# Performance work log

Hardware: AMD Instinct MI355X
Metric: run time of the kernel (lower is better)

## Reference

```python
import jax, jax.numpy as jnp
import numpy as np

K = 16  # neighbors
EPS = 1e-5

def conv1x1(x, w):
    # x: (B,C,N,1), w: (O,C) -> (B,O,N,1)
    return jnp.einsum('oc,bcnw->bonw', w, x)

def batch_norm(x, gamma, beta):
    # training-mode BatchNorm2d: biased batch stats over (B,N,W)
    mean = jnp.mean(x, axis=(0, 2, 3), keepdims=True)
    var = jnp.var(x, axis=(0, 2, 3), keepdims=True)
    xn = (x - mean) * jax.lax.rsqrt(var + EPS)
    return xn * gamma[None, :, None, None] + beta[None, :, None, None]

def gelu(x):
    return jax.nn.gelu(x, approximate=False)  # torch exact GELU

def knn_idx(x, k):
    # x: (B,C,N,1) -> neighbor indices (B,N,k), no grad (detach in torch)
    feat = jnp.squeeze(x, -1).transpose(0, 2, 1)  # (B,N,C)
    sq = jnp.sum(feat * feat, axis=-1)            # (B,N)
    dist = sq[:, :, None] - 2.0 * jnp.einsum('bnc,bmc->bnm', feat, feat) + sq[:, None, :]
    _, idx = jax.lax.top_k(-dist, k)              # nearest k (B,N,k)
    return idx

def mr_conv(x, idx, w, b, gamma, beta):
    # MRConv2d: x_j = gather neighbors, aggregate max(x_j - x_i), interleave channels, 1x1 conv + BN + GELU
    B, C, N, _ = x.shape
    feat = jnp.squeeze(x, -1)  # (B,C,N)
    # x_j[b,c,n,m] = feat[b,c,idx[b,n,m]]
    x_j = jax.vmap(lambda f, i: f[:, i])(feat, idx)      # (B,C,N,k)
    agg = jnp.max(x_j - feat[:, :, :, None], axis=-1)    # (B,C,N)
    # cat([x.unsqueeze(2), x_j.unsqueeze(2)], dim=2).reshape(B, 2C, N, 1) -> interleaved channels
    h = jnp.stack([feat, agg], axis=2).reshape(B, 2 * C, N)[..., None]  # (B,2C,N,1)
    h = jnp.einsum('oc,bcnw->bonw', w, h) + b[None, :, None, None]
    return gelu(batch_norm(h, gamma, beta))

def setup_inputs() -> dict:
    key = jax.random.key(0)
    ks = jax.random.split(key, 5)
    B, C, N = 4, 192, 4096
    s = 1.0 / np.sqrt(C)
    return {
        'x': jax.random.normal(ks[0], (B, C, N, 1), jnp.float32),
        'w_fc1': jax.random.normal(ks[1], (C, C), jnp.float32) * s,
        'w_fc2': jax.random.normal(ks[2], (C, C), jnp.float32) * s,
        'w_mr': jax.random.normal(ks[3], (C, 2 * C), jnp.float32) * (1.0 / np.sqrt(2 * C)),
        'b_mr': jnp.zeros((C,), jnp.float32),
        'g0': jnp.ones((C,), jnp.float32), 'b0': jnp.zeros((C,), jnp.float32),
        'gm': jnp.ones((C,), jnp.float32), 'bm': jnp.zeros((C,), jnp.float32),
        'g1': jnp.ones((C,), jnp.float32), 'b1': jnp.zeros((C,), jnp.float32),
    }

def reference(x, w_fc1, w_fc2, w_mr, b_mr, g0, b0, gm, bm, g1, b1):
    inp = x
    h = batch_norm(conv1x1(x, w_fc1), g0, b0)
    idx = knn_idx(jax.lax.stop_gradient(h), K)
    h = mr_conv(h, idx, w_mr, b_mr, gm, bm)
    h = batch_norm(gelu(h), g1, b1)
    h = conv1x1(h, w_fc2)
    return h + inp
```

## Files before the change

### kernel.cpp

```cpp
#include <hip/hip_runtime.h>
#include <hip/hip_bf16.h>
#include <math.h>

#define BSZ 4
#define NPT 4096
#define CH  192
#define KNB 16
#define KPH 16
#define KCAND (2 * KPH)
#define NTOT ((float)(BSZ * NPT))
#define NT64 ((double)(BSZ * NPT))

typedef short short8 __attribute__((ext_vector_type(8)));
typedef float f32x4  __attribute__((ext_vector_type(4)));

__device__ __forceinline__ float gelu_exact(float x){
    return 0.5f * x * (1.0f + erff(x * 0.70710678118654752440f));
}
__device__ __forceinline__ unsigned int umin_(unsigned int a, unsigned int b){ return a < b ? a : b; }
__device__ __forceinline__ unsigned int umax_(unsigned int a, unsigned int b){ return a < b ? b : a; }
__device__ __forceinline__ unsigned int umed3_(unsigned int a, unsigned int b, unsigned int c){
    unsigned int r;
    asm("v_med3_u32 %0, %1, %2, %3" : "=v"(r) : "v"(a), "v"(b), "v"(c));
    return r;
}
__device__ __forceinline__ unsigned short bf16rnd(float v){
    unsigned int bits = __builtin_bit_cast(unsigned int, v);
    return (unsigned short)((bits + 0x7fff + ((bits >> 16) & 1)) >> 16);
}

__global__ __launch_bounds__(256) void k_fc1_f64(
    const float* __restrict__ in, const float* __restrict__ W, double* __restrict__ outd,
    double* __restrict__ s0sum, double* __restrict__ s0sq)
{
    constexpr int OT = 8, NT = 4;
    __shared__ float wtT[CH][OT];
    __shared__ double redS[4][8], redQ[4][8];
    const int tid = threadIdx.x;
    const int o0  = blockIdx.y * OT;
    const int b   = blockIdx.z;
    const int n   = blockIdx.x * (256 * NT) + tid * NT;

    for (int lin = tid; lin < CH * OT; lin += 256){
        int c = lin >> 3, o = lin & 7;
        wtT[c][o] = W[(size_t)(o0 + o) * CH + c];
    }
    __syncthreads();

    double acc[OT][NT] = {};
    const float* ip = in + (size_t)b * CH * NPT + n;
    for (int c = 0; c < CH; ++c){
        float4 x4 = *reinterpret_cast<const float4*>(ip + (size_t)c * NPT);
        double xv[NT] = {x4.x, x4.y, x4.z, x4.w};
        float4 w0 = *reinterpret_cast<const float4*>(&wtT[c][0]);
        float4 w1 = *reinterpret_cast<const float4*>(&wtT[c][4]);
        double wv[OT] = {w0.x, w0.y, w0.z, w0.w, w1.x, w1.y, w1.z, w1.w};
        #pragma unroll
        for (int oo = 0; oo < OT; ++oo)
            #pragma unroll
            for (int j = 0; j < NT; ++j)
                acc[oo][j] = fma(wv[oo], xv[j], acc[oo][j]);
    }

    double ps[OT], pq[OT];
    #pragma unroll
    for (int oo = 0; oo < OT; ++oo){
        size_t off = ((size_t)b * CH + o0 + oo) * NPT + n;
        double s = 0., q = 0.;
        #pragma unroll
        for (int j = 0; j < 4; ++j){
            double v = acc[oo][j];
            outd[off + j] = v;
            s += v; q = fma(v, v, q);
        }
        ps[oo] = s; pq[oo] = q;
    }

    #pragma unroll
    for (int oo = 0; oo < OT; ++oo){
        #pragma unroll
        for (int off = 32; off; off >>= 1){
            ps[oo] += __shfl_xor(ps[oo], off);
            pq[oo] += __shfl_xor(pq[oo], off);
        }
    }
    const int wv = tid >> 6, lane = tid & 63;
    if (lane == 0){
        #pragma unroll
        for (int oo = 0; oo < OT; ++oo){ redS[wv][oo] = ps[oo]; redQ[wv][oo] = pq[oo]; }
    }
    __syncthreads();
    if (tid < 8){
        double s = redS[0][tid] + redS[1][tid] + redS[2][tid] + redS[3][tid];
        double q = redQ[0][tid] + redQ[1][tid] + redQ[2][tid] + redQ[3][tid];
        atomicAdd(&s0sum[o0 + tid], s);
        atomicAdd(&s0sq[o0 + tid], q);
    }
}

__global__ void k_feat(
    const double* __restrict__ t1d, const float* __restrict__ g0,
    const double* __restrict__ s0sum, const double* __restrict__ s0sq,
    double* __restrict__ featT, float* __restrict__ feat32,
    unsigned short* __restrict__ featP, float* __restrict__ sqv)
{
    __shared__ double tile[32][33];
    __shared__ float sqp[32][33];
    __shared__ double scdl[CH];
    const int n0 = blockIdx.x * 32, b = blockIdx.y;
    const int tx = threadIdx.x, ty = threadIdx.y;
    const int tid = ty * 32 + tx;
    float part[4] = {0.f, 0.f, 0.f, 0.f};
    unsigned short* fpb = featP + (size_t)b * NPT * CH;

    for (int i = tid; i < CH; i += 256){
        double mean = s0sum[i] / NT64;
        double var  = s0sq[i] / NT64 - mean * mean;
        scdl[i] = (1.0 / sqrt(var + 1e-5)) * (double)g0[i];
    }
    __syncthreads();

    for (int cc = 0; cc < CH / 32; ++cc){
        const int cbase = cc * 32;
        #pragma unroll
        for (int r = 0; r < 32; r += 8){
            int c = cbase + ty + r;
            tile[ty + r][tx] = t1d[((size_t)b * CH + c) * NPT + n0 + tx] * scdl[c];
        }
        __syncthreads();
        #pragma unroll
        for (int r = 0; r < 32; r += 8){
            int n = n0 + ty + r;
            int c = cbase + tx;
            double v = tile[tx][ty + r];
            size_t o = ((size_t)b * NPT + n) * CH + c;
            featT[o] = v;
            float f = (float)v;
            feat32[o] = f;
            part[r >> 3] = fmaf(f, f, part[r >> 3]);
        }
        if (tid < 128){
            const int t_ = tid >> 6;
            const int l  = tid & 63;
            const int r_ = l & 15, g_ = l >> 4;
            const int nl = t_ * 16 + r_;
            short8 pk;
            #pragma unroll
            for (int e = 0; e < 8; ++e)
                pk[e] = (short)bf16rnd((float)tile[g_ * 8 + e][nl]);
            const int tP = blockIdx.x * 2 + t_;
            *reinterpret_cast<short8*>(fpb + (size_t)(tP * 6 + cc) * 512 + l * 8) = pk;
        }
        __syncthreads();
    }
    #pragma unroll
    for (int j = 0; j < 4; ++j) sqp[ty + 8 * j][tx] = part[j];
    __syncthreads();
    if (ty == 0){
        float s = 0.f;
        #pragma unroll 8
        for (int k = 0; k < 32; ++k) s += sqp[tx][k];
        sqv[b * NPT + n0 + tx] = s;
    }
}

__global__ __launch_bounds__(1024, 8) void k_knn_mfma(
    const unsigned short* __restrict__ featP, const float* __restrict__ sqv,
    int* __restrict__ idxh)
{
    __shared__ unsigned int mlist[16][16][17];
    const int tid  = threadIdx.x;
    const int wv   = tid >> 6;
    const int lane = tid & 63;
    const int r = lane & 15, g = lane >> 4;
    const int b    = blockIdx.y;
    const int qt   = blockIdx.x >> 1;
    const int half = blockIdx.x & 1;
    const int qs = wv >> 2, me = wv & 3;
    const int tq   = qt * 4 + qs;
    const int tm0  = half * 128 + me * 32;
    const unsigned short* fp = featP + (size_t)b * NPT * CH;

    short8 bq0, bq1, bq2, bq3, bq4, bq5;
    {
        const unsigned short* qp = fp + (size_t)tq * 3072 + lane * 8;
        bq0 = *reinterpret_cast<const short8*>(qp);
        bq1 = *reinterpret_cast<const short8*>(qp + 512);
        bq2 = *reinterpret_cast<const short8*>(qp + 1024);
        bq3 = *reinterpret_cast<const short8*>(qp + 1536);
        bq4 = *reinterpret_cast<const short8*>(qp + 2048);
        bq5 = *reinterpret_cast<const short8*>(qp + 2560);
    }

    unsigned int Q[16];
    #pragma unroll
    for (int e = 0; e < 16; ++e) Q[e] = 0xFFFFFFFFu;

    const float* sq = sqv + b * NPT;
    const unsigned short* pa = fp + (size_t)tm0 * 3072 + lane * 8;

    for (int it = 0; it < 32; ++it){
        const unsigned short* p = pa + (size_t)it * 3072;
        short8 a0 = *reinterpret_cast<const short8*>(p);
        short8 a1 = *reinterpret_cast<const short8*>(p + 512);
        short8 a2 = *reinterpret_cast<const short8*>(p + 1024);
        short8 a3 = *reinterpret_cast<const short8*>(p + 1536);
        short8 a4 = *reinterpret_cast<const short8*>(p + 2048);
        short8 a5 = *reinterpret_cast<const short8*>(p + 2560);
        const int tm = tm0 + it;
        float4 s4 = *reinterpret_cast<const float4*>(sq + tm * 16 + 4 * g);

        f32x4 acc = {0.f, 0.f, 0.f, 0.f};
        acc = __builtin_amdgcn_mfma_f32_16x16x32_bf16(a0, bq0, acc, 0, 0, 0);
        acc = __builtin_amdgcn_mfma_f32_16x16x32_bf16(a1, bq1, acc, 0, 0, 0);
        acc = __builtin_amdgcn_mfma_f32_16x16x32_bf16(a2, bq2, acc, 0, 0, 0);
        acc = __builtin_amdgcn_mfma_f32_16x16x32_bf16(a3, bq3, acc, 0, 0, 0);
        acc = __builtin_amdgcn_mfma_f32_16x16x32_bf16(a4, bq4, acc, 0, 0, 0);
        acc = __builtin_amdgcn_mfma_f32_16x16x32_bf16(a5, bq5, acc, 0, 0, 0);

        const int m0 = tm * 16 + 4 * g;
        float sa[4] = {s4.x, s4.y, s4.z, s4.w};
        #pragma unroll
        for (int u = 0; u < 4; ++u){
            float d = fmaxf(fmaf(-2.0f, acc[u], sa[u]), 0.0f);
            unsigned int k = (__builtin_bit_cast(unsigned int, d) & 0xFFFFF000u)
                           | (unsigned int)(m0 + u);
            #pragma unroll
            for (int pz = 0; pz < 8; ++pz){
                unsigned int a = Q[2 * pz], bv = Q[2 * pz + 1];
                Q[2 * pz]     = umin_(a, k);
                Q[2 * pz + 1] = umed3_(a, bv, k);
                k             = umax_(bv, k);
            }
        }
    }

    #pragma unroll 1
    for (int rd = 0; rd < 16; ++rd){
        unsigned int v = Q[0];
        v = umin_(v, (unsigned int)__shfl_xor((int)v, 16));
        v = umin_(v, (unsigned int)__shfl_xor((int)v, 32));
        bool win = (Q[0] == v);
        if (win){
            #pragma unroll
            for (int e = 0; e < 15; ++e) Q[e] = Q[e + 1];
            Q[15] = 0xFFFFFFFFu;
        }
        if (g == 0) mlist[wv][r][rd] = v;
    }
    if (g == 0) mlist[wv][r][16] = 0xFFFFFFFFu;
    __syncthreads();

    if (tid < 64){
        const int qq = tid;
        const int q2 = qq >> 4, rr = qq & 15;
        int i0 = 0, i1 = 0, i2 = 0, i3 = 0;
        int* op = idxh + ((size_t)(b * NPT + qt * 64 + qq) * 2 + half) * KPH;
        for (int rd = 0; rd < KPH; ++rd){
            unsigned int k0 = mlist[q2 * 4 + 0][rr][i0];
            unsigned int k1 = mlist[q2 * 4 + 1][rr][i1];
            unsigned int k2 = mlist[q2 * 4 + 2][rr][i2];
            unsigned int k3 = mlist[q2 * 4 + 3][rr][i3];
            unsigned int mm = umin_(umin_(k0, k1), umin_(k2, k3));
            op[rd] = (int)(mm & 0xFFFu);
            i0 += (k0 == mm); i1 += (k1 == mm); i2 += (k2 == mm); i3 += (k3 == mm);
        }
    }
}

__global__ __launch_bounds__(256) void k_refine(
    const float* __restrict__ feat32, const double* __restrict__ featT,
    const int* __restrict__ idxh, int* __restrict__ idxf)
{
    const int q = blockIdx.x * 8 + (threadIdx.x >> 5);
    const int b = blockIdx.y;
    const int sl = threadIdx.x & 31;
    const int* cl = idxh + ((size_t)b * NPT + q) * KCAND;
    const float* qv = feat32 + ((size_t)b * NPT + q) * CH;
    float qr[6];
    #pragma unroll
    for (int j = 0; j < 6; ++j) qr[j] = qv[sl + 32 * j];

    float myd = INFINITY; int mym = 0x7fffffff;
    #pragma unroll
    for (int t0 = 0; t0 < KCAND; t0 += 8){
        float pd[8]; int cm[8];
        #pragma unroll
        for (int j = 0; j < 8; ++j){
            int m = cl[t0 + j];
            cm[j] = m;
            const float* cv = feat32 + ((size_t)b * NPT + m) * CH;
            float d = 0.f;
            #pragma unroll
            for (int e = 0; e < 6; ++e){
                float dv = cv[sl + 32 * e] - qr[e];
                d = fmaf(dv, dv, d);
            }
            pd[j] = d;
        }
        #pragma unroll
        for (int j = 0; j < 8; ++j){
            float d = pd[j];
            #pragma unroll
            for (int off = 16; off; off >>= 1) d += __shfl_xor(d, off, 32);
            if (sl == t0 + j){ myd = d; mym = cm[j]; }
        }
    }

    float d16 = 0.f;
    for (int r = 0; r < KNB; ++r){
        float bv = myd; int bi = mym;
        #pragma unroll
        for (int off = 16; off; off >>= 1){
            float ov = __shfl_xor(bv, off, 32);
            int   oi = __shfl_xor(bi, off, 32);
            if (ov < bv || (ov == bv && oi < bi)){ bv = ov; bi = oi; }
        }
        if (sl == 0) idxf[((size_t)b * NPT + q) * KNB + r] = bi;
        if (mym == bi){ myd = INFINITY; mym = 0x7fffffff; }
        d16 = bv;
    }
    float b17 = myd;
    #pragma unroll
    for (int off = 16; off; off >>= 1) b17 = fminf(b17, __shfl_xor(b17, off, 32));
    int flag = (b17 - d16 < 1e-3f + 2e-4f * d16) ? 1 : 0;
    flag = __shfl(flag, 0, 32);
    if (!flag) return;

    const double* qvd = featT + ((size_t)b * NPT + q) * CH;
    double qrd[6];
    #pragma unroll
    for (int j = 0; j < 6; ++j) qrd[j] = qvd[sl + 32 * j];
    double mydd = INFINITY; int mymd = 0x7fffffff;
    for (int t = 0; t < KCAND; ++t){
        int m = cl[t];
        const double* cv = featT + ((size_t)b * NPT + m) * CH;
        double d = 0.;
        #pragma unroll
        for (int e = 0; e < 6; ++e){
            double dv = cv[sl + 32 * e] - qrd[e];
            d = fma(dv, dv, d);
        }
        #pragma unroll
        for (int off = 16; off; off >>= 1) d += __shfl_xor(d, off, 32);
        if (sl == t){ mydd = d; mymd = m; }
    }
    for (int r = 0; r < KNB; ++r){
        double bv = mydd; int bi = mymd;
        #pragma unroll
        for (int off = 16; off; off >>= 1){
            double ov = __shfl_xor(bv, off, 32);
            int    oi = __shfl_xor(bi, off, 32);
            if (ov < bv || (ov == bv && oi < bi)){ bv = ov; bi = oi; }
        }
        if (sl == 0) idxf[((size_t)b * NPT + q) * KNB + r] = bi;
        if (mymd == bi){ mydd = INFINITY; mymd = 0x7fffffff; }
    }
}

__global__ __launch_bounds__(128) void k_gather2(
    const float* __restrict__ feat32, const float* __restrict__ g0,
    const float* __restrict__ b0, const double* __restrict__ s0sum,
    const double* __restrict__ s0sq, const int* __restrict__ idx,
    unsigned short* __restrict__ hfrag)
{
    __shared__ float lt[192 * 33];
    __shared__ int il[32 * KNB];
    __shared__ float shl[CH];
    const int tid = threadIdx.x;
    const int n0  = blockIdx.x * 32;
    const int cg  = blockIdx.y;
    const int b   = blockIdx.z;

    for (int i = tid; i < 32 * KNB; i += 128)
        il[i] = idx[((size_t)b * NPT + n0) * KNB + i];
    for (int i = tid; i < CH; i += 128){
        double mean = s0sum[i] / NT64;
        double var  = s0sq[i] / NT64 - mean * mean;
        double sc   = (1.0 / sqrt(var + 1e-5)) * (double)g0[i];
        shl[i] = (float)((double)b0[i] - mean * sc);
    }
    __syncthreads();

    const int nl = tid >> 2, sub = tid & 3;
    const int n  = n0 + nl;
    const float* fbase = feat32 + (size_t)b * NPT * CH;
    const float* qr = fbase + (size_t)n * CH + cg * 96;

    float4 qv[6], mx[6];
    #pragma unroll
    for (int j = 0; j < 6; ++j){
        qv[j] = *reinterpret_cast<const float4*>(qr + (sub + 4 * j) * 4);
        mx[j] = make_float4(-INFINITY, -INFINITY, -INFINITY, -INFINITY);
    }

    #pragma unroll 4
    for (int k = 0; k < KNB; ++k){
        const float* cr = fbase + (size_t)il[nl * KNB + k] * CH + cg * 96;
        #pragma unroll
        for (int j = 0; j < 6; ++j){
            float4 v = *reinterpret_cast<const float4*>(cr + (sub + 4 * j) * 4);
            mx[j].x = fmaxf(mx[j].x, v.x - qv[j].x);
            mx[j].y = fmaxf(mx[j].y, v.y - qv[j].y);
            mx[j].z = fmaxf(mx[j].z, v.z - qv[j].z);
            mx[j].w = fmaxf(mx[j].w, v.w - qv[j].w);
        }
    }

    #pragma unroll
    for (int j = 0; j < 6; ++j){
        const int cb = (sub + 4 * j) * 4;
        float4 s4 = *reinterpret_cast<const float4*>(&shl[cg * 96 + cb]);
        float fi[4] = {qv[j].x + s4.x, qv[j].y + s4.y, qv[j].z + s4.z, qv[j].w + s4.w};
        float mm[4] = {mx[j].x, mx[j].y, mx[j].z, mx[j].w};
        #pragma unroll
        for (int e = 0; e < 4; ++e){
            int cl = cb + e;
            lt[(2 * cl) * 33 + nl]     = fi[e];
            lt[(2 * cl + 1) * 33 + nl] = mm[e];
        }
    }
    __syncthreads();

    const int jt0 = (b * NPT + n0) >> 4;
    const int wvv = tid >> 6;
    const int l   = tid & 63;
    for (int p = wvv; p < 12; p += 2){
        const int t_ = p & 1, ksl = p >> 1;
        short8 pk;
        #pragma unroll
        for (int e = 0; e < 8; ++e){
            int ic = ksl * 32 + (l >> 4) * 8 + e;
            pk[e] = (short)bf16rnd(lt[ic * 33 + t_ * 16 + (l & 15)]);
        }
        *reinterpret_cast<short8*>(
            &hfrag[((size_t)(jt0 + t_) * 12 + cg * 6 + ksl) * 512 + l * 8]) = pk;
    }
}

__global__ __launch_bounds__(64) void k_wprep(
    const float* __restrict__ wmr, unsigned short* __restrict__ wfrag)
{
    const int ot = blockIdx.x, ks = blockIdx.y, l = threadIdx.x;
    short8 pk;
    #pragma unroll
    for (int e = 0; e < 8; ++e)
        pk[e] = (short)bf16rnd(wmr[(size_t)(ot * 16 + (l & 15)) * (2 * CH) + ks * 32 + (l >> 4) * 8 + e]);
    *reinterpret_cast<short8*>(&wfrag[((size_t)ot * 12 + ks) * 512 + l * 8]) = pk;
}

__global__ __launch_bounds__(256) void k_gemm_mr(
    const unsigned short* __restrict__ hfrag, const unsigned short* __restrict__ wfrag,
    const float* __restrict__ bias, float* __restrict__ out,
    float* __restrict__ s1sum, float* __restrict__ s1sq)
{
    __shared__ unsigned short hl[4 * 12 * 512];
    __shared__ unsigned short wl[12 * 512];
    __shared__ float sstat[2 * CH];
    const int tid = threadIdx.x;
    const int wv = tid >> 6, lane = tid & 63;
    const int g = lane >> 4;
    const int j0 = blockIdx.x * 64;
    const int b  = j0 >> 12;
    const int n0 = j0 & (NPT - 1);

    const unsigned short* hsrc = hfrag + (size_t)(j0 >> 4) * 12 * 512;
    for (int i = tid; i < 3072; i += 256)
        *reinterpret_cast<short8*>(&hl[i * 8]) = *reinterpret_cast<const short8*>(&hsrc[i * 8]);
    for (int i = tid; i < 2 * CH; i += 256) sstat[i] = 0.f;
    __syncthreads();

    for (int ot = 0; ot < 12; ++ot){
        for (int i = tid; i < 768; i += 256)
            *reinterpret_cast<short8*>(&wl[i * 8]) =
                *reinterpret_cast<const short8*>(&wfrag[((size_t)ot * 12) * 512 + i * 8]);
        __syncthreads();

        f32x4 acc = {0.f, 0.f, 0.f, 0.f};
        #pragma unroll
        for (int ks = 0; ks < 12; ++ks){
            short8 a = *reinterpret_cast<const short8*>(&wl[ks * 512 + lane * 8]);
            short8 h = *reinterpret_cast<const short8*>(&hl[(wv * 12 + ks) * 512 + lane * 8]);
            acc = __builtin_amdgcn_mfma_f32_16x16x32_bf16(a, h, acc, 0, 0, 0);
        }

        #pragma unroll
        for (int u = 0; u < 4; ++u){
            const int row = ot * 16 + 4 * g + u;
            float val = acc[u] + bias[row];
            out[((size_t)b * CH + row) * NPT + n0 + wv * 16 + (lane & 15)] = val;
            float s = val, q = val * val;
            #pragma unroll
            for (int off = 1; off < 16; off <<= 1){
                s += __shfl_xor(s, off, 16);
                q += __shfl_xor(q, off, 16);
            }
            if ((lane & 15) == 0){
                atomicAdd(&sstat[row], s);
                atomicAdd(&sstat[CH + row], q);
            }
        }
        __syncthreads();
    }

    if (tid < CH){
        atomicAdd(&s1sum[tid], sstat[tid]);
        atomicAdd(&s1sq[tid],  sstat[CH + tid]);
    }
}

__global__ __launch_bounds__(256) void k_u(
    const float* __restrict__ in, const float* __restrict__ s1sum, const float* __restrict__ s1sq,
    const float* __restrict__ gm, const float* __restrict__ bm,
    float* __restrict__ out, float* __restrict__ s2sum, float* __restrict__ s2sq)
{
    __shared__ float redS[4], redQ[4];
    const int c = blockIdx.y, b = blockIdx.z;
    const int n = (blockIdx.x * 256 + threadIdx.x) * 4;
    const float invn = 1.0f / NTOT;
    float mean = s1sum[c] * invn;
    float var  = s1sq[c] * invn - mean * mean;
    float rstd = rsqrtf(var + 1e-5f);
    float s = rstd * gm[c], t = bm[c] - mean * s;

    size_t i = ((size_t)b * CH + c) * NPT + n;
    float4 v = *reinterpret_cast<const float4*>(in + i);
    float4 o;
    o.x = gelu_exact(gelu_exact(fmaf(v.x, s, t)));
    o.y = gelu_exact(gelu_exact(fmaf(v.y, s, t)));
    o.z = gelu_exact(gelu_exact(fmaf(v.z, s, t)));
    o.w = gelu_exact(gelu_exact(fmaf(v.w, s, t)));
    *reinterpret_cast<float4*>(out + i) = o;

    float ps = o.x + o.y + o.z + o.w;
    float pq = fmaf(o.x, o.x, fmaf(o.y, o.y, fmaf(o.z, o.z, o.w * o.w)));
    #pragma unroll
    for (int off = 32; off; off >>= 1){
        ps += __shfl_xor(ps, off);
        pq += __shfl_xor(pq, off);
    }
    const int wv = threadIdx.x >> 6, lane = threadIdx.x & 63;
    if (lane == 0){ redS[wv] = ps; redQ[wv] = pq; }
    __syncthreads();
    if (threadIdx.x == 0){
        atomicAdd(&s2sum[c], redS[0] + redS[1] + redS[2] + redS[3]);
        atomicAdd(&s2sq[c],  redQ[0] + redQ[1] + redQ[2] + redQ[3]);
    }
}

__global__ __launch_bounds__(256) void k_gemm_fc2(
    const float* __restrict__ in, const float* __restrict__ W,
    const float* __restrict__ s2sum, const float* __restrict__ s2sq,
    const float* __restrict__ g1, const float* __restrict__ b1,
    const float* __restrict__ resid, float* __restrict__ out)
{
    constexpr int KDIM = CH, OT = 8, NT = 4;
    __shared__ float wtT[KDIM][OT];
    __shared__ float scl[KDIM], shl[KDIM];
    const int tid = threadIdx.x;
    const int o0  = blockIdx.y * OT;
    const int b   = blockIdx.z;
    const int n   = blockIdx.x * (256 * NT) + tid * NT;

    for (int lin = tid; lin < KDIM * OT; lin += 256){
        int c = lin >> 3, o = lin & 7;
        wtT[c][o] = W[(size_t)(o0 + o) * KDIM + c];
    }
    const float invn = 1.0f / NTOT;
    for (int c = tid; c < KDIM; c += 256){
        float mean = s2sum[c] * invn;
        float var  = s2sq[c] * invn - mean * mean;
        float rstd = rsqrtf(var + 1e-5f);
        float s = rstd * g1[c];
        scl[c] = s;
        shl[c] = b1[c] - mean * s;
    }
    __syncthreads();

    float acc[OT][NT] = {};
    const float* ip = in + (size_t)b * KDIM * NPT + n;
    #pragma unroll 2
    for (int c = 0; c < KDIM; ++c){
        float4 x4 = *reinterpret_cast<const float4*>(ip + (size_t)c * NPT);
        float xv[NT];
        xv[0] = fmaf(x4.x, scl[c], shl[c]);
        xv[1] = fmaf(x4.y, scl[c], shl[c]);
        xv[2] = fmaf(x4.z, scl[c], shl[c]);
        xv[3] = fmaf(x4.w, scl[c], shl[c]);
        float4 w0 = *reinterpret_cast<const float4*>(&wtT[c][0]);
        float4 w1 = *reinterpret_cast<const float4*>(&wtT[c][4]);
        float wv[OT] = {w0.x, w0.y, w0.z, w0.w, w1.x, w1.y, w1.z, w1.w};
        #pragma unroll
        for (int oo = 0; oo < OT; ++oo)
            #pragma unroll
            for (int j = 0; j < NT; ++j)
                acc[oo][j] = fmaf(wv[oo], xv[j], acc[oo][j]);
    }

    #pragma unroll
    for (int oo = 0; oo < OT; ++oo){
        size_t off = ((size_t)b * CH + o0 + oo) * NPT + n;
        float4 r4 = *reinterpret_cast<const float4*>(resid + off);
        float4 o4;
        o4.x = acc[oo][0] + r4.x; o4.y = acc[oo][1] + r4.y;
        o4.z = acc[oo][2] + r4.z; o4.w = acc[oo][3] + r4.w;
        *reinterpret_cast<float4*>(out + off) = o4;
    }
}

extern "C" void kernel_launch(void* const* d_in, const int* in_sizes, int n_in,
                              void* d_out, int out_size, void* d_ws, size_t ws_size,
                              hipStream_t stream)
{
    const float* x    = (const float*)d_in[0];
    const float* w1   = (const float*)d_in[1];
    const float* w2   = (const float*)d_in[2];
    const float* wmr  = (const float*)d_in[3];
    const float* bmr  = (const float*)d_in[4];
    const float* g0   = (const float*)d_in[5];
    const float* b0   = (const float*)d_in[6];
    const float* gm   = (const float*)d_in[7];
    const float* bm   = (const float*)d_in[8];
    const float* g1   = (const float*)d_in[9];
    const float* b1   = (const float*)d_in[10];
    float* outp = (float*)d_out;

    const size_t BCN = (size_t)BSZ * CH * NPT;
    float*  A      = (float*)d_ws;
    float*  Bb     = A + BCN;
    unsigned short* featP = (unsigned short*)Bb;
    float*  Cc     = Bb + BCN;
    double* t1d    = (double*)Cc;
    unsigned short* hfrag = (unsigned short*)Cc;
    double* featT  = (double*)(Cc + 2 * BCN);
    float*  feat32 = (float*)(featT + BCN);
    float*  sqv    = feat32 + BCN;
    int*    idxh   = (int*)(sqv + (size_t)BSZ * NPT);
    int*    idxf   = idxh + (size_t)BSZ * NPT * KCAND;
    float*  bnacc  = (float*)(idxf + (size_t)BSZ * NPT * KNB);
    float *s1sum = bnacc, *s1sq = bnacc + CH, *s2sum = bnacc + 2 * CH, *s2sq = bnacc + 3 * CH;
    double* s0sum  = (double*)(bnacc + 4 * CH);
    double* s0sq   = s0sum + CH;
    unsigned short* wfrag = (unsigned short*)(s0sq + CH);

    dim3 gg(NPT / 1024, CH / 8, BSZ);
    dim3 ge(NPT / 1024, CH, BSZ);

    hipMemsetAsync(bnacc, 0, 4 * CH * sizeof(float) + 2 * CH * sizeof(double), stream);
    k_wprep<<<dim3(12, 12), 64, 0, stream>>>(wmr, wfrag);
    k_fc1_f64<<<gg, 256, 0, stream>>>(x, w1, t1d, s0sum, s0sq);
    k_feat<<<dim3(NPT / 32, BSZ), dim3(32, 8), 0, stream>>>(t1d, g0, s0sum, s0sq,
                                                            featT, feat32, featP, sqv);
    k_knn_mfma<<<dim3(2 * NPT / 64, BSZ), 1024, 0, stream>>>(featP, sqv, idxh);
    k_refine<<<dim3(NPT / 8, BSZ), 256, 0, stream>>>(feat32, featT, idxh, idxf);
    k_gather2<<<dim3(NPT / 32, 2, BSZ), 128, 0, stream>>>(feat32, g0, b0, s0sum, s0sq, idxf, hfrag);
    k_gemm_mr<<<dim3(BSZ * NPT / 64), 256, 0, stream>>>(hfrag, wfrag, bmr, A, s1sum, s1sq);
    k_u<<<ge, 256, 0, stream>>>(A, s1sum, s1sq, gm, bm, Bb, s2sum, s2sq);
    k_gemm_fc2<<<gg, 256, 0, stream>>>(Bb, w2, s2sum, s2sq, g1, b1, x, outp);
}
```

Measured before the change: 336.3 us.

## Move fc2 GEMM to bf16 MFMA with BN folded into weights and bias

The elementwise GELU/BN kernel now transposes tiles through shared memory and writes bf16 MFMA fragments instead of fp32 activations. The final BatchNorm is folded into the fc2 weights (scaled per input channel) plus a precomputed output bias. The fc2 GEMM then runs on 16x16x32 bf16 MFMA instructions rather than scalar fp32 FMAs. This cuts memory traffic and FMA cost but lowers the fc2 input precision to bf16 and adds two small prep kernels.

```diff
diff --git a/kernel.cpp b/kernel.cpp
--- a/kernel.cpp
+++ b/kernel.cpp
@@ -510,101 +510,143 @@
 }
 
 __global__ __launch_bounds__(256) void k_u(
-    const float* __restrict__ in, const float* __restrict__ s1sum, const float* __restrict__ s1sq,
+    const float* __restrict__ t2, const float* __restrict__ s1sum, const float* __restrict__ s1sq,
     const float* __restrict__ gm, const float* __restrict__ bm,
-    float* __restrict__ out, float* __restrict__ s2sum, float* __restrict__ s2sq)
-{
-    __shared__ float redS[4], redQ[4];
-    const int c = blockIdx.y, b = blockIdx.z;
-    const int n = (blockIdx.x * 256 + threadIdx.x) * 4;
+    unsigned short* __restrict__ ufrag, float* __restrict__ s2sum, float* __restrict__ s2sq)
+{
+    __shared__ float lt[CH * 33];
+    __shared__ float sstatS[CH], sstatQ[CH];
+    __shared__ float scl1[CH], shl1[CH];
+    const int tid = threadIdx.x;
+    const int n0 = blockIdx.x * 32;
+    const int b  = blockIdx.y;
     const float invn = 1.0f / NTOT;
-    float mean = s1sum[c] * invn;
-    float var  = s1sq[c] * invn - mean * mean;
-    float rstd = rsqrtf(var + 1e-5f);
-    float s = rstd * gm[c], t = bm[c] - mean * s;
-
-    size_t i = ((size_t)b * CH + c) * NPT + n;
-    float4 v = *reinterpret_cast<const float4*>(in + i);
-    float4 o;
-    o.x = gelu_exact(gelu_exact(fmaf(v.x, s, t)));
-    o.y = gelu_exact(gelu_exact(fmaf(v.y, s, t)));
-    o.z = gelu_exact(gelu_exact(fmaf(v.z, s, t)));
-    o.w = gelu_exact(gelu_exact(fmaf(v.w, s, t)));
-    *reinterpret_cast<float4*>(out + i) = o;
-
-    float ps = o.x + o.y + o.z + o.w;
-    float pq = fmaf(o.x, o.x, fmaf(o.y, o.y, fmaf(o.z, o.z, o.w * o.w)));
-    #pragma unroll
-    for (int off = 32; off; off >>= 1){
-        ps += __shfl_xor(ps, off);
-        pq += __shfl_xor(pq, off);
-    }
-    const int wv = threadIdx.x >> 6, lane = threadIdx.x & 63;
-    if (lane == 0){ redS[wv] = ps; redQ[wv] = pq; }
-    __syncthreads();
-    if (threadIdx.x == 0){
-        atomicAdd(&s2sum[c], redS[0] + redS[1] + redS[2] + redS[3]);
-        atomicAdd(&s2sq[c],  redQ[0] + redQ[1] + redQ[2] + redQ[3]);
-    }
-}
-
-__global__ __launch_bounds__(256) void k_gemm_fc2(
-    const float* __restrict__ in, const float* __restrict__ W,
-    const float* __restrict__ s2sum, const float* __restrict__ s2sq,
-    const float* __restrict__ g1, const float* __restrict__ b1,
-    const float* __restrict__ resid, float* __restrict__ out)
-{
-    constexpr int KDIM = CH, OT = 8, NT = 4;
-    __shared__ float wtT[KDIM][OT];
-    __shared__ float scl[KDIM], shl[KDIM];
-    const int tid = threadIdx.x;
-    const int o0  = blockIdx.y * OT;
-    const int b   = blockIdx.z;
-    const int n   = blockIdx.x * (256 * NT) + tid * NT;
-
-    for (int lin = tid; lin < KDIM * OT; lin += 256){
-        int c = lin >> 3, o = lin & 7;
-        wtT[c][o] = W[(size_t)(o0 + o) * KDIM + c];
-    }
+    for (int c = tid; c < CH; c += 256){
+        float mean = s1sum[c] * invn;
+        float var  = s1sq[c] * invn - mean * mean;
+        float rstd = rsqrtf(var + 1e-5f);
+        float s = rstd * gm[c];
+        scl1[c] = s; shl1[c] = bm[c] - mean * s;
+        sstatS[c] = 0.f; sstatQ[c] = 0.f;
+    }
+    __syncthreads();
+
+    for (int i = tid; i < CH * 32; i += 256){
+        int c = i >> 5, nl = i & 31;
+        float v = t2[((size_t)b * CH + c) * NPT + n0 + nl];
+        float uv = gelu_exact(gelu_exact(fmaf(v, scl1[c], shl1[c])));
+        lt[c * 33 + nl] = uv;
+        float s = uv, q = uv * uv;
+        #pragma unroll
+        for (int off = 16; off; off >>= 1){
+            s += __shfl_xor(s, off, 32);
+            q += __shfl_xor(q, off, 32);
+        }
+        if ((tid & 31) == 0){
+            atomicAdd(&sstatS[c], s);
+            atomicAdd(&sstatQ[c], q);
+        }
+    }
+    __syncthreads();
+
+    const int jt0 = (b * NPT + n0) >> 4;
+    const int wvv = tid >> 6, l = tid & 63;
+    for (int p = wvv; p < 12; p += 4){
+        const int t_ = p & 1, ksl = p >> 1;
+        short8 pk;
+        #pragma unroll
+        for (int e = 0; e < 8; ++e){
+            int c = ksl * 32 + (l >> 4) * 8 + e;
+            pk[e] = (short)bf16rnd(lt[c * 33 + t_ * 16 + (l & 15)]);
+        }
+        *reinterpret_cast<short8*>(&ufrag[((size_t)(jt0 + t_) * 6 + ksl) * 512 + l * 8]) = pk;
+    }
+
+    if (tid < CH){
+        atomicAdd(&s2sum[tid], sstatS[tid]);
+        atomicAdd(&s2sq[tid],  sstatQ[tid]);
+    }
+}
+
+__global__ __launch_bounds__(64) void k_w2prep(
+    const float* __restrict__ w2, const float* __restrict__ s2sum, const float* __restrict__ s2sq,
+    const float* __restrict__ g1, unsigned short* __restrict__ wfrag2)
+{
+    const int ot = blockIdx.x, ks = blockIdx.y, l = threadIdx.x;
     const float invn = 1.0f / NTOT;
-    for (int c = tid; c < KDIM; c += 256){
+    short8 pk;
+    #pragma unroll
+    for (int e = 0; e < 8; ++e){
+        int c = ks * 32 + (l >> 4) * 8 + e;
         float mean = s2sum[c] * invn;
         float var  = s2sq[c] * invn - mean * mean;
-        float rstd = rsqrtf(var + 1e-5f);
-        float s = rstd * g1[c];
-        scl[c] = s;
-        shl[c] = b1[c] - mean * s;
-    }
-    __syncthreads();
-
-    float acc[OT][NT] = {};
-    const float* ip = in + (size_t)b * KDIM * NPT + n;
-    #pragma unroll 2
-    for (int c = 0; c < KDIM; ++c){
-        float4 x4 = *reinterpret_cast<const float4*>(ip + (size_t)c * NPT);
-        float xv[NT];
-        xv[0] = fmaf(x4.x, scl[c], shl[c]);
-        xv[1] = fmaf(x4.y, scl[c], shl[c]);
-        xv[2] = fmaf(x4.z, scl[c], shl[c]);
-        xv[3] = fmaf(x4.w, scl[c], shl[c]);
-        float4 w0 = *reinterpret_cast<const float4*>(&wtT[c][0]);
-        float4 w1 = *reinterpret_cast<const float4*>(&wtT[c][4]);
-        float wv[OT] = {w0.x, w0.y, w0.z, w0.w, w1.x, w1.y, w1.z, w1.w};
-        #pragma unroll
-        for (int oo = 0; oo < OT; ++oo)
-            #pragma unroll
-            for (int j = 0; j < NT; ++j)
-                acc[oo][j] = fmaf(wv[oo], xv[j], acc[oo][j]);
-    }
-
-    #pragma unroll
-    for (int oo = 0; oo < OT; ++oo){
-        size_t off = ((size_t)b * CH + o0 + oo) * NPT + n;
-        float4 r4 = *reinterpret_cast<const float4*>(resid + off);
-        float4 o4;
-        o4.x = acc[oo][0] + r4.x; o4.y = acc[oo][1] + r4.y;
-        o4.z = acc[oo][2] + r4.z; o4.w = acc[oo][3] + r4.w;
-        *reinterpret_cast<float4*>(out + off) = o4;
+        float scl  = rsqrtf(var + 1e-5f) * g1[c];
+        pk[e] = (short)bf16rnd(w2[(size_t)(ot * 16 + (l & 15)) * CH + c] * scl);
+    }
+    *reinterpret_cast<short8*>(&wfrag2[((size_t)ot * 6 + ks) * 512 + l * 8]) = pk;
+}
+
+__global__ __launch_bounds__(256) void k_bias2(
+    const float* __restrict__ w2, const float* __restrict__ s2sum, const float* __restrict__ s2sq,
+    const float* __restrict__ g1, const float* __restrict__ b1, float* __restrict__ bias2)
+{
+    __shared__ float shl[CH];
+    const int tid = threadIdx.x;
+    const float invn = 1.0f / NTOT;
+    for (int c = tid; c < CH; c += 256){
+        float mean = s2sum[c] * invn;
+        float var  = s2sq[c] * invn - mean * mean;
+        float scl  = rsqrtf(var + 1e-5f) * g1[c];
+        shl[c] = b1[c] - mean * scl;
+    }
+    __syncthreads();
+    if (tid < CH){
+        float s = 0.f;
+        for (int c = 0; c < CH; ++c)
+            s = fmaf(w2[(size_t)tid * CH + c], shl[c], s);
+        bias2[tid] = s;
+    }
+}
+
+__global__ __launch_bounds__(256) void k_gemm_fc2(
+    const unsigned short* __restrict__ ufrag, const unsigned short* __restrict__ wfrag2,
+    const float* __restrict__ bias2, const float* __restrict__ resid, float* __restrict__ out)
+{
+    __shared__ unsigned short hl[4 * 6 * 512];
+    __shared__ unsigned short wl[6 * 512];
+    const int tid = threadIdx.x;
+    const int wv = tid >> 6, lane = tid & 63;
+    const int g = lane >> 4;
+    const int j0 = blockIdx.x * 64;
+    const int b  = j0 >> 12;
+    const int n0 = j0 & (NPT - 1);
+
+    const unsigned short* hsrc = ufrag + (size_t)(j0 >> 4) * 6 * 512;
+    for (int i = tid; i < 1536; i += 256)
+        *reinterpret_cast<short8*>(&hl[i * 8]) = *reinterpret_cast<const short8*>(&hsrc[i * 8]);
+    __syncthreads();
+
+    for (int ot = 0; ot < 12; ++ot){
+        for (int i = tid; i < 384; i += 256)
+            *reinterpret_cast<short8*>(&wl[i * 8]) =
+                *reinterpret_cast<const short8*>(&wfrag2[((size_t)ot * 6) * 512 + i * 8]);
+        __syncthreads();
+
+        f32x4 acc = {0.f, 0.f, 0.f, 0.f};
+        #pragma unroll
+        for (int ks = 0; ks < 6; ++ks){
+            short8 a = *reinterpret_cast<const short8*>(&wl[ks * 512 + lane * 8]);
+            short8 h = *reinterpret_cast<const short8*>(&hl[(wv * 6 + ks) * 512 + lane * 8]);
+            acc = __builtin_amdgcn_mfma_f32_16x16x32_bf16(a, h, acc, 0, 0, 0);
+        }
+
+        #pragma unroll
+        for (int u = 0; u < 4; ++u){
+            const int row = ot * 16 + 4 * g + u;
+            size_t off = ((size_t)b * CH + row) * NPT + n0 + wv * 16 + (lane & 15);
+            out[off] = acc[u] + bias2[row] + resid[off];
+        }
+        __syncthreads();
     }
 }
 
@@ -629,6 +671,7 @@
     float*  A      = (float*)d_ws;
     float*  Bb     = A + BCN;
     unsigned short* featP = (unsigned short*)Bb;
+    unsigned short* ufrag = (unsigned short*)Bb;
     float*  Cc     = Bb + BCN;
     double* t1d    = (double*)Cc;
     unsigned short* hfrag = (unsigned short*)Cc;
@@ -641,10 +684,11 @@
     float *s1sum = bnacc, *s1sq = bnacc + CH, *s2sum = bnacc + 2 * CH, *s2sq = bnacc + 3 * CH;
     double* s0sum  = (double*)(bnacc + 4 * CH);
     double* s0sq   = s0sum + CH;
-    unsigned short* wfrag = (unsigned short*)(s0sq + CH);
+    unsigned short* wfrag  = (unsigned short*)(s0sq + CH);
+    unsigned short* wfrag2 = wfrag + 12 * 12 * 512;
+    float* bias2 = (float*)(wfrag2 + 12 * 6 * 512);
 
     dim3 gg(NPT / 1024, CH / 8, BSZ);
-    dim3 ge(NPT / 1024, CH, BSZ);
 
     hipMemsetAsync(bnacc, 0, 4 * CH * sizeof(float) + 2 * CH * sizeof(double), stream);
     k_wprep<<<dim3(12, 12), 64, 0, stream>>>(wmr, wfrag);
@@ -655,6 +699,8 @@
     k_refine<<<dim3(NPT / 8, BSZ), 256, 0, stream>>>(feat32, featT, idxh, idxf);
     k_gather2<<<dim3(NPT / 32, 2, BSZ), 128, 0, stream>>>(feat32, g0, b0, s0sum, s0sq, idxf, hfrag);
     k_gemm_mr<<<dim3(BSZ * NPT / 64), 256, 0, stream>>>(hfrag, wfrag, bmr, A, s1sum, s1sq);
-    k_u<<<ge, 256, 0, stream>>>(A, s1sum, s1sq, gm, bm, Bb, s2sum, s2sq);
-    k_gemm_fc2<<<gg, 256, 0, stream>>>(Bb, w2, s2sum, s2sq, g1, b1, x, outp);
-}
+    k_u<<<dim3(NPT / 32, BSZ), 256, 0, stream>>>(A, s1sum, s1sq, gm, bm, ufrag, s2sum, s2sq);
+    k_w2prep<<<dim3(12, 6), 64, 0, stream>>>(w2, s2sum, s2sq, g1, wfrag2);
+    k_bias2<<<1, 256, 0, stream>>>(w2, s2sum, s2sq, g1, b1, bias2);
+    k_gemm_fc2<<<dim3(BSZ * NPT / 64), 256, 0, stream>>>(ufrag, wfrag2, bias2, x, outp);
+}
```

After: 333.4 us. Within noise of the previous version (-0.9%).
